# Kernel optimization log

Measured on AMD Instinct MI355X. Metric: run time of the kernel, lower is better.

The kernel has to match this reference:

```python
import jax, jax.numpy as jnp
import numpy as np

N = 50000
E = 800000
D_IN, D_HID, D_OUT = 128, 128, 40
K = 3  # TAGConv default hops


def setup_inputs() -> dict:
    key = jax.random.key(0)
    k1, k2, k3, k4, k5, k6 = jax.random.split(key, 6)
    x = jax.random.normal(k1, (N, D_IN), dtype=jnp.float32)
    edge_index = jax.random.randint(k2, (2, E), 0, N, dtype=jnp.int64)
    edge_weight = jnp.ones((E,), dtype=jnp.float32)
    s1 = 1.0 / np.sqrt(D_IN)
    s2 = 1.0 / np.sqrt(D_HID)
    W1 = jax.random.uniform(k3, (K + 1, D_IN, D_HID), jnp.float32, -s1, s1)
    b1 = jax.random.uniform(k4, (D_HID,), jnp.float32, -s1, s1)
    W2 = jax.random.uniform(k5, (K + 1, D_HID, D_OUT), jnp.float32, -s2, s2)
    b2 = jax.random.uniform(k6, (D_OUT,), jnp.float32, -s2, s2)
    return {"x": x, "edge_index": edge_index, "edge_weight": edge_weight,
            "W1": W1, "b1": b1, "W2": W2, "b2": b2}


def _gcn_norm(edge_index, edge_weight, num_nodes):
    # symmetric normalization, NO self-loops (TAGConv default)
    src, dst = edge_index[0], edge_index[1]
    deg = jax.ops.segment_sum(edge_weight, dst, num_segments=num_nodes)
    dis = jnp.where(deg > 0, jax.lax.rsqrt(jnp.where(deg > 0, deg, 1.0)), 0.0)
    return dis[src] * edge_weight * dis[dst]


def _tag_conv(x, src, dst, norm, W, b, num_nodes):
    # out = sum_{k=0..K} A_norm^k x @ W[k] + b
    out = x @ W[0]
    h = x
    for k in range(1, K + 1):
        h = jax.ops.segment_sum(norm[:, None] * h[src], dst, num_segments=num_nodes)
        out = out + h @ W[k]
    return out + b


def reference(x, edge_index, edge_weight, W1, b1, W2, b2):
    src, dst = edge_index[0], edge_index[1]
    norm = _gcn_norm(edge_index, edge_weight, N)
    h = jax.nn.relu(_tag_conv(x, src, dst, norm, W1, b1, N))
    # dropout is identity in eval mode
    out = _tag_conv(h, src, dst, norm, W2, b2, N)
    return jax.nn.log_softmax(out, axis=1)
```

## Files before the change

kernel.cpp:

```cpp
#include <hip/hip_runtime.h>
#include <hip/hip_bf16.h>
#include <hip/hip_fp16.h>


#define SLOTS 48

using half8 = __attribute__((ext_vector_type(8))) _Float16;
using f32x4 = __attribute__((ext_vector_type(4))) float;

__device__ __forceinline__ float2 rec_h2f(uint u) {
  union { uint u; __half2 h; } cv; cv.u = u;
  return __half22float2(cv.h);
}
__device__ __forceinline__ float rec_w(uint rec) {
  union { ushort s; __half h; } cv; cv.s = (ushort)(rec >> 16);
  return __half2float(cv.h);
}
__device__ __forceinline__ uint f2hbits(float f) {
  union { __half h; ushort s; } cv; cv.h = __float2half(f);
  return (uint)cv.s;
}
__device__ __forceinline__ uint h22u(__half2 h) {
  union { __half2 h; uint u; } cv; cv.h = h; return cv.u;
}

__global__ void scatter_kernel(const int* __restrict__ ei, const float* __restrict__ ew,
                               int* __restrict__ cnt, uint* __restrict__ es, int E) {
  int e = blockIdx.x * blockDim.x + threadIdx.x;
  if (e < E) {
    int s = ei[e];
    int d = ei[E + e];
    uint rec = (uint)s | (f2hbits(ew[e]) << 16);
    int pos = atomicAdd(&cnt[(size_t)d << 4], 1);
    if (pos < SLOTS) es[(size_t)d * SLOTS + pos] = rec;
  }
}

__global__ __launch_bounds__(256) void deg_kernel(const uint* __restrict__ es,
                                                  float* __restrict__ dis, int n) {
  int lane = threadIdx.x & 63;
  int node = blockIdx.x * 4 + (threadIdx.x >> 6);
  if (node >= n) return;
  float s = (lane < SLOTS) ? rec_w(es[(size_t)node * SLOTS + lane]) : 0.f;
  #pragma unroll
  for (int off = 32; off; off >>= 1) s += __shfl_xor(s, off);
  if (lane == 0) dis[node] = (s > 0.f) ? rsqrtf(s) : 0.f;
}

__global__ void xh_kernel(const float* __restrict__ x, __half* __restrict__ xh, int total4) {
  int i = blockIdx.x * blockDim.x + threadIdx.x;
  if (i < total4) {
    float4 v = ((const float4*)x)[i];
    __half2* o = (__half2*)xh;
    o[i * 2 + 0] = __floats2half2_rn(v.x, v.y);
    o[i * 2 + 1] = __floats2half2_rn(v.z, v.w);
  }
}

__global__ void wt_kernel(const float* __restrict__ W, __half* __restrict__ Wt,
                          int total, int cols, int incols) {
  int i = blockIdx.x * blockDim.x + threadIdx.x;
  if (i >= total) return;
  int kk = i & 127;
  int rem = i >> 7;
  int c = rem % cols;
  int s = rem / cols;
  float v = (c < incols) ? W[(size_t)s * 128 * incols + (size_t)kk * incols + c] : 0.f;
  Wt[i] = __float2half(v);
}

__global__ __launch_bounds__(256) void g128x4_kernel(const __half* __restrict__ Xh,
                                                     const __half* __restrict__ Wt,
                                                     const float* __restrict__ dis,
                                                     __half* __restrict__ Y0,
                                                     __half* __restrict__ Y1,
                                                     __half* __restrict__ Y2,
                                                     __half* __restrict__ Y3, int n) {
  __shared__ __align__(16) __half sX[64 * 128];
  __shared__ __align__(16) __half sW[128 * 128];
  int t = threadIdx.x;
  int row0 = blockIdx.x * 64;
  for (int c8 = t; c8 < 1024; c8 += 256) {
    int r = c8 >> 4, ck = c8 & 15;
    int gr = row0 + r;
    half8 v = {};
    if (gr < n) v = *(const half8*)&Xh[(size_t)gr * 128 + ck * 8];
    *(half8*)&sX[(r * 16 + (ck ^ (r & 7))) * 8] = v;
  }
  int w = t >> 6, lane = t & 63;
  int lrow = lane & 15, lk = lane >> 4;
  int ocol = lane & 15;
  int orow = (lane >> 4) * 4;
  half8 a[4];
  __half* outs[4] = {Y0, Y1, Y2, Y3};
  #pragma unroll
  for (int s = 0; s < 4; ++s) {
    __syncthreads();
    for (int c8 = t; c8 < 2048; c8 += 256) {
      int r = c8 >> 4, ck = c8 & 15;
      half8 v = *(const half8*)&Wt[(size_t)s * 16384 + c8 * 8];
      *(half8*)&sW[(r * 16 + (ck ^ (r & 7))) * 8] = v;
    }
    __syncthreads();
    if (s == 0) {
      int r = w * 16 + lrow;
      #pragma unroll
      for (int kk = 0; kk < 4; ++kk) {
        int ck = kk * 4 + lk;
        a[kk] = *(const half8*)&sX[(r * 16 + (ck ^ (r & 7))) * 8];
      }
    }
    #pragma unroll
    for (int ct = 0; ct < 8; ++ct) {
      f32x4 acc = (f32x4){0.f, 0.f, 0.f, 0.f};
      int c = ct * 16 + lrow;
      #pragma unroll
      for (int kk = 0; kk < 4; ++kk) {
        int ck = kk * 4 + lk;
        half8 b = *(const half8*)&sW[(c * 16 + (ck ^ (c & 7))) * 8];
        acc = __builtin_amdgcn_mfma_f32_16x16x32_f16(a[kk], b, acc, 0, 0, 0);
      }
      int oc = ct * 16 + ocol;
      #pragma unroll
      for (int rg = 0; rg < 4; ++rg) {
        int gr = row0 + w * 16 + orow + rg;
        if (gr < n) {
          float v = acc[rg];
          if (s == 3) v *= dis[gr];
          outs[s][(size_t)gr * 128 + oc] = __float2half(v);
        }
      }
    }
  }
}

__global__ __launch_bounds__(256) void g40x4_kernel(const __half* __restrict__ Xh,
                                                    const __half* __restrict__ Wt,
                                                    const float* __restrict__ dis,
                                                    __half* __restrict__ Z0,
                                                    __half* __restrict__ Z1,
                                                    __half* __restrict__ Z2,
                                                    __half* __restrict__ Z3, int n) {
  __shared__ __align__(16) __half sX[64 * 128];
  __shared__ __align__(16) __half sW[48 * 128];
  int t = threadIdx.x;
  int row0 = blockIdx.x * 64;
  for (int c8 = t; c8 < 1024; c8 += 256) {
    int r = c8 >> 4, ck = c8 & 15;
    int gr = row0 + r;
    half8 v = {};
    if (gr < n) v = *(const half8*)&Xh[(size_t)gr * 128 + ck * 8];
    *(half8*)&sX[(r * 16 + (ck ^ (r & 7))) * 8] = v;
  }
  int w = t >> 6, lane = t & 63;
  int lrow = lane & 15, lk = lane >> 4;
  int ocol = lane & 15;
  int orow = (lane >> 4) * 4;
  half8 a[4];
  __half* outs[4] = {Z0, Z1, Z2, Z3};
  #pragma unroll
  for (int s = 0; s < 4; ++s) {
    __syncthreads();
    for (int c8 = t; c8 < 768; c8 += 256) {
      int r = c8 >> 4, ck = c8 & 15;
      half8 v = *(const half8*)&Wt[(size_t)s * 6144 + c8 * 8];
      *(half8*)&sW[(r * 16 + (ck ^ (r & 7))) * 8] = v;
    }
    __syncthreads();
    if (s == 0) {
      int r = w * 16 + lrow;
      #pragma unroll
      for (int kk = 0; kk < 4; ++kk) {
        int ck = kk * 4 + lk;
        a[kk] = *(const half8*)&sX[(r * 16 + (ck ^ (r & 7))) * 8];
      }
    }
    #pragma unroll
    for (int ct = 0; ct < 3; ++ct) {
      f32x4 acc = (f32x4){0.f, 0.f, 0.f, 0.f};
      int c = ct * 16 + lrow;
      #pragma unroll
      for (int kk = 0; kk < 4; ++kk) {
        int ck = kk * 4 + lk;
        half8 b = *(const half8*)&sW[(c * 16 + (ck ^ (c & 7))) * 8];
        acc = __builtin_amdgcn_mfma_f32_16x16x32_f16(a[kk], b, acc, 0, 0, 0);
      }
      int oc = ct * 16 + ocol;
      if (oc >= 40) continue;
      #pragma unroll
      for (int rg = 0; rg < 4; ++rg) {
        int gr = row0 + w * 16 + orow + rg;
        if (gr < n) {
          float v = acc[rg];
          if (s == 3) v *= dis[gr];
          outs[s][(size_t)gr * 40 + oc] = __float2half(v);
        }
      }
    }
  }
}

__global__ __launch_bounds__(256) void prop128_kernel(const __half* __restrict__ srch,
                                                      __half* __restrict__ dsth,
                                                      const int* __restrict__ cnts,
                                                      const uint* __restrict__ es,
                                                      const float* __restrict__ dis,
                                                      const __half* __restrict__ Yadd,
                                                      const float* __restrict__ bias,
                                                      int finalRelu, int n) {
  int lane = threadIdx.x & 63;
  int node = blockIdx.x * 4 + (threadIdx.x >> 6);
  if (node >= n) return;
  int c = min(cnts[(size_t)node << 4], SLOTS);
  int nit = (c + 7) >> 3;
  const uint* ep = es + (size_t)node * SLOTS;
  const uint2* sf = (const uint2*)srch;
  int hi = lane >> 5;
  int fl = lane & 31;
  float ax = 0.f, ay = 0.f, az = 0.f, aw = 0.f;
  uint q0 = 0, q1 = 0, q2 = 0, q3 = 0;
  if (nit > 0) {
    const uint* p0 = ep + hi;
    q0 = p0[0]; q1 = p0[2]; q2 = p0[4]; q3 = p0[6];
  }
  for (int it = 0; it < nit; ++it) {
    uint n0 = q0, n1 = q1, n2 = q2, n3 = q3;
    if (it + 1 < nit) {
      const uint* np = ep + ((it + 1) << 3) + hi;
      n0 = np[0]; n1 = np[2]; n2 = np[4]; n3 = np[6];
    }
    uint2 g0 = sf[(q0 & 0xffffu) * 32u + fl];
    uint2 g1 = sf[(q1 & 0xffffu) * 32u + fl];
    uint2 g2 = sf[(q2 & 0xffffu) * 32u + fl];
    uint2 g3 = sf[(q3 & 0xffffu) * 32u + fl];
    float w0 = rec_w(q0), w1 = rec_w(q1), w2 = rec_w(q2), w3 = rec_w(q3);
    float2 p0a = rec_h2f(g0.x), p0b = rec_h2f(g0.y);
    float2 p1a = rec_h2f(g1.x), p1b = rec_h2f(g1.y);
    float2 p2a = rec_h2f(g2.x), p2b = rec_h2f(g2.y);
    float2 p3a = rec_h2f(g3.x), p3b = rec_h2f(g3.y);
    ax = fmaf(w0, p0a.x, ax); ay = fmaf(w0, p0a.y, ay);
    az = fmaf(w0, p0b.x, az); aw = fmaf(w0, p0b.y, aw);
    ax = fmaf(w1, p1a.x, ax); ay = fmaf(w1, p1a.y, ay);
    az = fmaf(w1, p1b.x, az); aw = fmaf(w1, p1b.y, aw);
    ax = fmaf(w2, p2a.x, ax); ay = fmaf(w2, p2a.y, ay);
    az = fmaf(w2, p2b.x, az); aw = fmaf(w2, p2b.y, aw);
    ax = fmaf(w3, p3a.x, ax); ay = fmaf(w3, p3a.y, ay);
    az = fmaf(w3, p3b.x, az); aw = fmaf(w3, p3b.y, aw);
    q0 = n0; q1 = n1; q2 = n2; q3 = n3;
  }
  ax += __shfl_xor(ax, 32); ay += __shfl_xor(ay, 32);
  az += __shfl_xor(az, 32); aw += __shfl_xor(aw, 32);
  if (hi == 0) {
    float dn = dis[node];
    uint2 yv = ((const uint2*)Yadd)[(size_t)node * 32 + fl];
    float2 y01 = rec_h2f(yv.x), y23 = rec_h2f(yv.y);
    float o0, o1, o2, o3;
    if (finalRelu) {
      o0 = fmaxf(y01.x + dn * ax + bias[fl * 4 + 0], 0.f);
      o1 = fmaxf(y01.y + dn * ay + bias[fl * 4 + 1], 0.f);
      o2 = fmaxf(y23.x + dn * az + bias[fl * 4 + 2], 0.f);
      o3 = fmaxf(y23.y + dn * aw + bias[fl * 4 + 3], 0.f);
    } else {
      o0 = dn * (y01.x + dn * ax);
      o1 = dn * (y01.y + dn * ay);
      o2 = dn * (y23.x + dn * az);
      o3 = dn * (y23.y + dn * aw);
    }
    uint2 o;
    o.x = h22u(__floats2half2_rn(o0, o1));
    o.y = h22u(__floats2half2_rn(o2, o3));
    ((uint2*)dsth)[(size_t)node * 32 + fl] = o;
  }
}

__global__ __launch_bounds__(256) void prop40_kernel(const __half* __restrict__ srch,
                                                     __half* __restrict__ dsth,
                                                     float* __restrict__ dstf,
                                                     const int* __restrict__ cnts,
                                                     const uint* __restrict__ es,
                                                     const float* __restrict__ dis,
                                                     const __half* __restrict__ Yadd,
                                                     int writeF32, int n) {
  int lane = threadIdx.x & 63;
  int node = blockIdx.x * 4 + (threadIdx.x >> 6);
  if (node >= n) return;
  int c = min(cnts[(size_t)node << 4], SLOTS);
  int nit = (c + 7) >> 3;
  const uint* ep = es + (size_t)node * SLOTS;
  const __half2* sf = (const __half2*)srch;
  int hi = lane >> 5;
  int fl = lane & 31;
  bool act = (fl < 20);
  float ax = 0.f, ay = 0.f;
  uint q0 = 0, q1 = 0, q2 = 0, q3 = 0;
  if (nit > 0) {
    const uint* p0 = ep + hi;
    q0 = p0[0]; q1 = p0[2]; q2 = p0[4]; q3 = p0[6];
  }
  for (int it = 0; it < nit; ++it) {
    uint n0 = q0, n1 = q1, n2 = q2, n3 = q3;
    if (it + 1 < nit) {
      const uint* np = ep + ((it + 1) << 3) + hi;
      n0 = np[0]; n1 = np[2]; n2 = np[4]; n3 = np[6];
    }
    uint i0 = act ? ((q0 & 0xffffu) * 20u + fl) : 0u;
    uint i1 = act ? ((q1 & 0xffffu) * 20u + fl) : 0u;
    uint i2 = act ? ((q2 & 0xffffu) * 20u + fl) : 0u;
    uint i3 = act ? ((q3 & 0xffffu) * 20u + fl) : 0u;
    float2 v0 = __half22float2(sf[i0]);
    float2 v1 = __half22float2(sf[i1]);
    float2 v2 = __half22float2(sf[i2]);
    float2 v3 = __half22float2(sf[i3]);
    float w0 = rec_w(q0), w1 = rec_w(q1), w2 = rec_w(q2), w3 = rec_w(q3);
    ax = fmaf(w0, v0.x, ax); ay = fmaf(w0, v0.y, ay);
    ax = fmaf(w1, v1.x, ax); ay = fmaf(w1, v1.y, ay);
    ax = fmaf(w2, v2.x, ax); ay = fmaf(w2, v2.y, ay);
    ax = fmaf(w3, v3.x, ax); ay = fmaf(w3, v3.y, ay);
    q0 = n0; q1 = n1; q2 = n2; q3 = n3;
  }
  ax += __shfl_xor(ax, 32);
  ay += __shfl_xor(ay, 32);
  if (hi == 0 && act) {
    float dn = dis[node];
    float2 y = __half22float2(((const __half2*)Yadd)[(size_t)node * 20 + fl]);
    if (writeF32) {
      float2 o = make_float2(y.x + dn * ax, y.y + dn * ay);
      ((float2*)dstf)[(size_t)node * 20 + fl] = o;
    } else {
      float o0 = dn * (y.x + dn * ax);
      float o1 = dn * (y.y + dn * ay);
      ((__half2*)dsth)[(size_t)node * 20 + fl] = __floats2half2_rn(o0, o1);
    }
  }
}

__global__ __launch_bounds__(256) void lsm_kernel(const float* __restrict__ Z,
                                                  const float* __restrict__ b,
                                                  float* __restrict__ out, int n) {
  int lane = threadIdx.x & 63;
  int node = blockIdx.x * 4 + (threadIdx.x >> 6);
  if (node >= n) return;
  float v = -1e30f;
  if (lane < 40) v = Z[(size_t)node * 40 + lane] + b[lane];
  float m = v;
  #pragma unroll
  for (int off = 32; off; off >>= 1) m = fmaxf(m, __shfl_xor(m, off));
  float ex = (lane < 40) ? __expf(v - m) : 0.f;
  float s = ex;
  #pragma unroll
  for (int off = 32; off; off >>= 1) s += __shfl_xor(s, off);
  if (lane < 40) out[(size_t)node * 40 + lane] = v - m - __logf(s);
}

extern "C" void kernel_launch(void* const* d_in, const int* in_sizes, int n_in,
                              void* d_out, int out_size, void* d_ws, size_t ws_size,
                              hipStream_t stream) {
  const float* x  = (const float*)d_in[0];
  const int*   ei = (const int*)d_in[1];
  const float* ew = (const float*)d_in[2];
  const float* W1 = (const float*)d_in[3];
  const float* b1 = (const float*)d_in[4];
  const float* W2 = (const float*)d_in[5];
  const float* b2 = (const float*)d_in[6];
  float* out = (float*)d_out;

  const int N = in_sizes[0] / 128;
  const int E = in_sizes[2];

  char* ws = (char*)d_ws;
  size_t off = 0;
  auto alloc = [&](size_t bytes) -> void* {
    off = (off + 255) & ~(size_t)255;
    void* p = ws + off;
    off += bytes;
    return p;
  };
  float*  dis  = (float*) alloc((size_t)N * 4);
  int*    cnt  = (int*)   alloc((size_t)N * 64);
  uint*   es   = (uint*)  alloc((size_t)N * SLOTS * 4);
  __half* Xh   = (__half*)alloc((size_t)N * 128 * 2);
  __half* Y0   = (__half*)alloc((size_t)N * 128 * 2);
  __half* Y1   = (__half*)alloc((size_t)N * 128 * 2);
  __half* Y2   = (__half*)alloc((size_t)N * 128 * 2);
  __half* Y3   = (__half*)alloc((size_t)N * 128 * 2);
  __half* S2   = (__half*)alloc((size_t)N * 128 * 2);
  __half* S3   = (__half*)alloc((size_t)N * 128 * 2);
  __half* Hh   = (__half*)alloc((size_t)N * 128 * 2);
  __half* Z0   = (__half*)alloc((size_t)N * 40 * 2);
  __half* Z1   = (__half*)alloc((size_t)N * 40 * 2);
  __half* Z2   = (__half*)alloc((size_t)N * 40 * 2);
  __half* Z3   = (__half*)alloc((size_t)N * 40 * 2);
  __half* T2   = (__half*)alloc((size_t)N * 40 * 2);
  __half* T3   = (__half*)alloc((size_t)N * 40 * 2);
  float*  Zf   = (float*) alloc((size_t)N * 40 * 4);
  __half* W1t  = (__half*)alloc((size_t)4 * 128 * 128 * 2);
  __half* W2t  = (__half*)alloc((size_t)4 * 48 * 128 * 2);
  (void)ws_size; (void)n_in; (void)out_size;

  int nb_e  = (E + 255) / 256;
  int nb_g  = (N + 63) / 64;
  int nb_p4 = (N + 3) / 4;

  hipMemsetAsync(cnt, 0, (size_t)N * 64, stream);
  hipMemsetAsync(es, 0, (size_t)N * SLOTS * 4, stream);
  scatter_kernel<<<nb_e, 256, 0, stream>>>(ei, ew, cnt, es, E);
  deg_kernel<<<nb_p4, 256, 0, stream>>>(es, dis, N);

  xh_kernel<<<(N * 32 + 255) / 256, 256, 0, stream>>>(x, Xh, N * 32);
  wt_kernel<<<(4 * 128 * 128 + 255) / 256, 256, 0, stream>>>(W1, W1t, 4 * 128 * 128, 128, 128);
  wt_kernel<<<(4 * 48 * 128 + 255) / 256, 256, 0, stream>>>(W2, W2t, 4 * 48 * 128, 48, 40);

  g128x4_kernel<<<nb_g, 256, 0, stream>>>(Xh, W1t, dis, Y0, Y1, Y2, Y3, N);
  prop128_kernel<<<nb_p4, 256, 0, stream>>>(Y3, S2, cnt, es, dis, Y2, nullptr, 0, N);
  prop128_kernel<<<nb_p4, 256, 0, stream>>>(S2, S3, cnt, es, dis, Y1, nullptr, 0, N);
  prop128_kernel<<<nb_p4, 256, 0, stream>>>(S3, Hh, cnt, es, dis, Y0, b1, 1, N);

  g40x4_kernel<<<nb_g, 256, 0, stream>>>(Hh, W2t, dis, Z0, Z1, Z2, Z3, N);
  prop40_kernel<<<nb_p4, 256, 0, stream>>>(Z3, T2, nullptr, cnt, es, dis, Z2, 0, N);
  prop40_kernel<<<nb_p4, 256, 0, stream>>>(T2, T3, nullptr, cnt, es, dis, Z1, 0, N);
  prop40_kernel<<<nb_p4, 256, 0, stream>>>(T3, nullptr, Zf, cnt, es, dis, Z0, 1, N);

  lsm_kernel<<<nb_p4, 256, 0, stream>>>(Zf, b2, out, N);
}
```

Before: 289.0 us.

## Bin edges by destination range before scattering into per-node slots

Replaces the single random-scatter edge kernel with a two-pass binning scheme. The first pass groups edges into 8 buckets by destination node range, using a shared-memory histogram and one global atomic per bucket. The second pass scatters each bucket with blocks interleaved across buckets, so the cnt/es atomics and writes stay within a smaller address range for better cache locality. This adds an extra pass and an intermediate buffer of about 9.6 MB. The fixed BCAP of 150000 per bucket could overflow on skewed destination distributions.

```diff
diff --git a/kernel.cpp b/kernel.cpp
--- a/kernel.cpp
+++ b/kernel.cpp
@@ -4,6 +4,8 @@
 
 
 #define SLOTS 48
+#define NBUCK 8
+#define BCAP  150000
 
 using half8 = __attribute__((ext_vector_type(8))) _Float16;
 using f32x4 = __attribute__((ext_vector_type(4))) float;
@@ -24,15 +26,58 @@
   union { __half2 h; uint u; } cv; cv.h = h; return cv.u;
 }
 
-__global__ void scatter_kernel(const int* __restrict__ ei, const float* __restrict__ ew,
-                               int* __restrict__ cnt, uint* __restrict__ es, int E) {
-  int e = blockIdx.x * blockDim.x + threadIdx.x;
-  if (e < E) {
-    int s = ei[e];
-    int d = ei[E + e];
-    uint rec = (uint)s | (f2hbits(ew[e]) << 16);
-    int pos = atomicAdd(&cnt[(size_t)d << 4], 1);
-    if (pos < SLOTS) es[(size_t)d * SLOTS + pos] = rec;
+__global__ __launch_bounds__(256) void binA_kernel(const int* __restrict__ ei,
+                                                   const float* __restrict__ ew,
+                                                   int2* __restrict__ bucket,
+                                                   int* __restrict__ bcur,
+                                                   int E, uint magic) {
+  __shared__ int hist[NBUCK], base_s[NBUCK], lpos[NBUCK];
+  int t = threadIdx.x;
+  if (t < NBUCK) { hist[t] = 0; lpos[t] = 0; }
+  __syncthreads();
+  int e0 = blockIdx.x * 512;
+  int e1 = min(e0 + 512, E);
+  int ea = e0 + t;
+  int eb = e0 + 256 + t;
+  int d0 = -1, d1 = -1; uint r0 = 0, r1 = 0; int b0 = 0, b1 = 0;
+  if (ea < e1) {
+    d0 = ei[E + ea];
+    r0 = (uint)ei[ea] | (f2hbits(ew[ea]) << 16);
+    b0 = (int)__umulhi((uint)d0, magic);
+    atomicAdd(&hist[b0], 1);
+  }
+  if (eb < e1) {
+    d1 = ei[E + eb];
+    r1 = (uint)ei[eb] | (f2hbits(ew[eb]) << 16);
+    b1 = (int)__umulhi((uint)d1, magic);
+    atomicAdd(&hist[b1], 1);
+  }
+  __syncthreads();
+  if (t < NBUCK) base_s[t] = atomicAdd(&bcur[t], hist[t]);
+  __syncthreads();
+  if (d0 >= 0) {
+    int p = base_s[b0] + atomicAdd(&lpos[b0], 1);
+    bucket[(size_t)b0 * BCAP + p] = make_int2(d0, (int)r0);
+  }
+  if (d1 >= 0) {
+    int p = base_s[b1] + atomicAdd(&lpos[b1], 1);
+    bucket[(size_t)b1 * BCAP + p] = make_int2(d1, (int)r1);
+  }
+}
+
+__global__ __launch_bounds__(256) void binB_kernel(const int2* __restrict__ bucket,
+                                                   const int* __restrict__ bsz,
+                                                   int* __restrict__ cnt,
+                                                   uint* __restrict__ es) {
+  int r = blockIdx.x & (NBUCK - 1);
+  int slot = blockIdx.x >> 3;
+  int nsl = gridDim.x >> 3;
+  int sz = bsz[r];
+  const int2* bp = bucket + (size_t)r * BCAP;
+  for (int i = slot * 256 + (int)threadIdx.x; i < sz; i += nsl * 256) {
+    int2 p = bp[i];
+    int pos = atomicAdd(&cnt[(size_t)p.x << 4], 1);
+    if (pos < SLOTS) es[(size_t)p.x * SLOTS + pos] = (uint)p.y;
   }
 }
 
@@ -366,6 +411,7 @@
 
   const int N = in_sizes[0] / 128;
   const int E = in_sizes[2];
+  const uint magic = (uint)((((unsigned long long)NBUCK) << 32) / (unsigned long long)N + 1);
 
   char* ws = (char*)d_ws;
   size_t off = 0;
@@ -375,35 +421,39 @@
     off += bytes;
     return p;
   };
-  float*  dis  = (float*) alloc((size_t)N * 4);
-  int*    cnt  = (int*)   alloc((size_t)N * 64);
-  uint*   es   = (uint*)  alloc((size_t)N * SLOTS * 4);
-  __half* Xh   = (__half*)alloc((size_t)N * 128 * 2);
-  __half* Y0   = (__half*)alloc((size_t)N * 128 * 2);
-  __half* Y1   = (__half*)alloc((size_t)N * 128 * 2);
-  __half* Y2   = (__half*)alloc((size_t)N * 128 * 2);
-  __half* Y3   = (__half*)alloc((size_t)N * 128 * 2);
-  __half* S2   = (__half*)alloc((size_t)N * 128 * 2);
-  __half* S3   = (__half*)alloc((size_t)N * 128 * 2);
-  __half* Hh   = (__half*)alloc((size_t)N * 128 * 2);
-  __half* Z0   = (__half*)alloc((size_t)N * 40 * 2);
-  __half* Z1   = (__half*)alloc((size_t)N * 40 * 2);
-  __half* Z2   = (__half*)alloc((size_t)N * 40 * 2);
-  __half* Z3   = (__half*)alloc((size_t)N * 40 * 2);
-  __half* T2   = (__half*)alloc((size_t)N * 40 * 2);
-  __half* T3   = (__half*)alloc((size_t)N * 40 * 2);
-  float*  Zf   = (float*) alloc((size_t)N * 40 * 4);
-  __half* W1t  = (__half*)alloc((size_t)4 * 128 * 128 * 2);
-  __half* W2t  = (__half*)alloc((size_t)4 * 48 * 128 * 2);
+  float*  dis    = (float*) alloc((size_t)N * 4);
+  int*    cnt    = (int*)   alloc((size_t)N * 64);
+  int*    bcur   = (int*)   alloc((size_t)NBUCK * 4);
+  int2*   bucket = (int2*)  alloc((size_t)NBUCK * BCAP * 8);
+  uint*   es     = (uint*)  alloc((size_t)N * SLOTS * 4);
+  __half* Xh     = (__half*)alloc((size_t)N * 128 * 2);
+  __half* Y0     = (__half*)alloc((size_t)N * 128 * 2);
+  __half* Y1     = (__half*)alloc((size_t)N * 128 * 2);
+  __half* Y2     = (__half*)alloc((size_t)N * 128 * 2);
+  __half* Y3     = (__half*)alloc((size_t)N * 128 * 2);
+  __half* S2     = (__half*)alloc((size_t)N * 128 * 2);
+  __half* S3     = (__half*)alloc((size_t)N * 128 * 2);
+  __half* Hh     = (__half*)alloc((size_t)N * 128 * 2);
+  __half* Z0     = (__half*)alloc((size_t)N * 40 * 2);
+  __half* Z1     = (__half*)alloc((size_t)N * 40 * 2);
+  __half* Z2     = (__half*)alloc((size_t)N * 40 * 2);
+  __half* Z3     = (__half*)alloc((size_t)N * 40 * 2);
+  __half* T2     = (__half*)alloc((size_t)N * 40 * 2);
+  __half* T3     = (__half*)alloc((size_t)N * 40 * 2);
+  float*  Zf     = (float*) alloc((size_t)N * 40 * 4);
+  __half* W1t    = (__half*)alloc((size_t)4 * 128 * 128 * 2);
+  __half* W2t    = (__half*)alloc((size_t)4 * 48 * 128 * 2);
   (void)ws_size; (void)n_in; (void)out_size;
 
-  int nb_e  = (E + 255) / 256;
   int nb_g  = (N + 63) / 64;
   int nb_p4 = (N + 3) / 4;
+  int nb_bA = (E + 511) / 512;
 
   hipMemsetAsync(cnt, 0, (size_t)N * 64, stream);
+  hipMemsetAsync(bcur, 0, (size_t)NBUCK * 4, stream);
   hipMemsetAsync(es, 0, (size_t)N * SLOTS * 4, stream);
-  scatter_kernel<<<nb_e, 256, 0, stream>>>(ei, ew, cnt, es, E);
+  binA_kernel<<<nb_bA, 256, 0, stream>>>(ei, ew, bucket, bcur, E, magic);
+  binB_kernel<<<2048, 256, 0, stream>>>(bucket, bcur, cnt, es);
   deg_kernel<<<nb_p4, 256, 0, stream>>>(es, dis, N);
 
   xh_kernel<<<(N * 32 + 255) / 256, 256, 0, stream>>>(x, Xh, N * 32);
```

Result: slower. 300.3 us (+3.9%).
